# Optimization experiments

Measured on AMD Instinct MI355X. Metric: run time of the kernel, lower is better.

Reference implementation:

```python
import jax, jax.numpy as jnp
import numpy as np

T, B, C = 1024, 16, 1024
H, K, PAD = 16, 7, 6  # num_heads, kernel_size, padding_l (causal)
R = C // H


def setup_inputs() -> dict:
    key = jax.random.key(0)
    kx, kw = jax.random.split(key)
    x = jax.random.normal(kx, (T, B, C), dtype=jnp.float32)
    # xavier_uniform for weight_linear.weight of shape (H*K, C)
    bound = float(np.sqrt(6.0 / (C + H * K)))
    W = jax.random.uniform(kw, (H * K, C), dtype=jnp.float32, minval=-bound, maxval=bound)
    return {"x": x, "W": W}


def reference(x, W):
    Tn, Bn, Cn = x.shape
    # dynamic per-position conv weights: (T, B, H, K)
    w = jnp.einsum('tbc,oc->tbo', x, W).reshape(Tn, Bn, H, K)

    # band structure: row t attends absolute positions t + k - PAD, k in [0, K)
    pos = jnp.arange(Tn)[:, None] + jnp.arange(K)[None, :] - PAD     # (T, K)
    valid = (pos >= 0) & (pos < Tn)                                   # (T, K)
    logits = jnp.where(valid[:, None, None, :], w, -jnp.inf)
    wsm = jax.nn.softmax(logits, axis=-1)                             # (T, B, H, K), zeros off-band

    # windowed weighted sum (the bmm against the band matrix, done directly)
    pc = jnp.clip(pos, 0, Tn - 1)                                     # (T, K)
    xh = x.reshape(Tn, Bn, H, R)
    xg = xh[pc]                                                       # (T, K, B, H, R)
    out = jnp.einsum('tbhk,tkbhr->tbhr', wsm, xg).reshape(Tn, Bn, Cn)

    # dense (B*H, T, T) softmaxed band matrix, as returned by the torch module
    w_bht = wsm.transpose(1, 2, 0, 3).reshape(Bn * H, Tn, K)
    dense = jnp.zeros((Bn * H, Tn, Tn), wsm.dtype)
    dense = dense.at[:, jnp.arange(Tn)[:, None], pc].add(jnp.where(valid, w_bht, 0.0))
    return out, dense
```

## Files before the change

kernel.cpp:

```cpp
#include <hip/hip_runtime.h>
#include <math.h>

#define TT 1024
#define BB 16
#define CC 1024
#define HH 16
#define KK 7
#define PADL 6
#define HK 112
#define LSTRIDE 116

typedef short bf16x8 __attribute__((ext_vector_type(8)));
typedef float f32x4 __attribute__((ext_vector_type(4)));

__device__ __forceinline__ short f2bf(float f) {
    union { float f; unsigned u; } v; v.f = f;
    unsigned r = v.u + 0x7fff + ((v.u >> 16) & 1);
    return (short)(r >> 16);
}

__global__ __launch_bounds__(256) void k0_cvtW(const float* __restrict__ W,
                                               short* __restrict__ Wb) {
    const int i = (blockIdx.x * 256 + threadIdx.x) * 8;
    const float4 a0 = *(const float4*)(W + i);
    const float4 a1 = *(const float4*)(W + i + 4);
    bf16x8 v;
    v[0] = f2bf(a0.x); v[1] = f2bf(a0.y); v[2] = f2bf(a0.z); v[3] = f2bf(a0.w);
    v[4] = f2bf(a1.x); v[5] = f2bf(a1.y); v[6] = f2bf(a1.z); v[7] = f2bf(a1.w);
    *(bf16x8*)(Wb + i) = v;
}

__global__ __launch_bounds__(256) void k1_mfma(const float* __restrict__ x,
                                               const short* __restrict__ Wb,
                                               float* __restrict__ wsm) {
    __shared__ __align__(16) float Llog[4][16 * LSTRIDE];
    __shared__ __align__(16) float Lout[4][16 * HK];

    const int tid = threadIdx.x;
    const int w = tid >> 6;
    const int lane = tid & 63;
    const int quad = lane >> 4;
    const int lr = lane & 15;
    const int strip = blockIdx.x * 4 + w;
    const int r0 = strip * 16;

    bf16x8 ap, bp;
#pragma unroll
    for (int e = 0; e < 8; ++e) {
        const int k = quad * 8 + e;
        ap[e] = (k == lr) ? (short)0x3F80 : (short)0;
        bp[e] = f2bf((float)k);
    }
    f32x4 pz = (f32x4){0.f, 0.f, 0.f, 0.f};
    pz = __builtin_amdgcn_mfma_f32_16x16x32_bf16(ap, bp, pz, 0, 0, 0);
    const bool claim = (pz[0] == (float)(quad * 4)) &&
                       (pz[1] == (float)(quad * 4 + 1));

    const float* __restrict__ xa = x + (size_t)(r0 + lr) * CC + quad * 8;
    const short* __restrict__ wb = Wb + (size_t)lr * CC + quad * 8;

    f32x4 acc[7];
#pragma unroll
    for (int j = 0; j < 7; ++j) acc[j] = (f32x4){0.f, 0.f, 0.f, 0.f};

#pragma unroll 4
    for (int k0 = 0; k0 < CC; k0 += 32) {
        const float4 a0 = *(const float4*)(xa + k0);
        const float4 a1 = *(const float4*)(xa + k0 + 4);
        bf16x8 af;
        af[0] = f2bf(a0.x); af[1] = f2bf(a0.y); af[2] = f2bf(a0.z); af[3] = f2bf(a0.w);
        af[4] = f2bf(a1.x); af[5] = f2bf(a1.y); af[6] = f2bf(a1.z); af[7] = f2bf(a1.w);
#pragma unroll
        for (int j = 0; j < 7; ++j) {
            const bf16x8 bfrag = *(const bf16x8*)(wb + (size_t)(j * 16) * CC + k0);
            acc[j] = __builtin_amdgcn_mfma_f32_16x16x32_bf16(af, bfrag, acc[j], 0, 0, 0);
        }
    }

#pragma unroll
    for (int j = 0; j < 7; ++j)
#pragma unroll
        for (int r = 0; r < 4; ++r) {
            const int rowi = claim ? (quad * 4 + r) : lr;
            const int coli = claim ? lr : (quad * 4 + r);
            Llog[w][rowi * LSTRIDE + j * 16 + coli] = acc[j][r];
        }
    __syncthreads();

    const int kmin = (strip >= PADL) ? 0 : (PADL - strip);
#pragma unroll
    for (int p = 0; p < 4; ++p) {
        const int idx = p * 64 + lane;
        const int m = idx >> 4;
        const int h = idx & 15;
        const float* lp = &Llog[w][m * LSTRIDE + h * KK];
        float a[KK];
#pragma unroll
        for (int k = 0; k < KK; ++k) a[k] = lp[k];

        float mx = -INFINITY;
#pragma unroll
        for (int k = 0; k < KK; ++k)
            if (k >= kmin) mx = fmaxf(mx, a[k]);
        float e[KK], s = 0.f;
#pragma unroll
        for (int k = 0; k < KK; ++k) {
            if (k >= kmin) { e[k] = expf(a[k] - mx); s += e[k]; }
            else           { e[k] = 0.f; }
        }
        const float inv = 1.f / s;
        float* op = &Lout[w][m * HK + h * KK];
#pragma unroll
        for (int k = 0; k < KK; ++k) op[k] = e[k] * inv;
    }
    __syncthreads();

    float* __restrict__ dst = wsm + (size_t)r0 * HK;
    const float* __restrict__ src = &Lout[w][0];
#pragma unroll
    for (int i = 0; i < 7; ++i) {
        const int o = i * 256 + lane * 4;
        *(float4*)(dst + o) = *(const float4*)(src + o);
    }
}

__global__ __launch_bounds__(256) void k23_fused(const float* __restrict__ x,
                                                 const float* __restrict__ wsm,
                                                 float* __restrict__ dense,
                                                 float* __restrict__ out) {
    const int tid = threadIdx.x;
    const int base = blockIdx.x * 10;

    for (int it = 0; it < 10; ++it) {
        const int blk = base + it;

        if ((blk % 5) == 0) {
            const int r0 = (blk / 5) << 2;
            const int t = r0 >> 4;
            const int c = tid << 2;
            const int h = c >> 6;
            const int kmin = (t >= PADL) ? 0 : (PADL - t);

#pragma unroll
            for (int i = 0; i < 4; ++i) {
                const int row = r0 + i;
                const float* __restrict__ wp =
                    wsm + ((size_t)row * HH + h) * KK;
                float w[KK];
#pragma unroll
                for (int k = 0; k < KK; ++k) w[k] = wp[k];

                f32x4 acc = (f32x4){0.f, 0.f, 0.f, 0.f};
                for (int k = kmin; k < KK; ++k) {
                    const f32x4 xv = *(const f32x4*)(
                        x + ((size_t)row + (size_t)(k - PADL) * BB) * CC + c);
                    acc[0] += w[k] * xv[0];
                    acc[1] += w[k] * xv[1];
                    acc[2] += w[k] * xv[2];
                    acc[3] += w[k] * xv[3];
                }
                __builtin_nontemporal_store(acc,
                    (f32x4*)(out + (size_t)row * CC + c));
            }
        } else {
            const int blk2 = blk - (blk / 5) - 1;
            const int bh = blk2 >> 6;
            const int tc = blk2 & 63;
            const int b = bh >> 4;
            const int h = bh & 15;
            const int t0 = tc * 16;

            const int col = tid << 2;
            float* __restrict__ drow =
                dense + ((size_t)bh * TT + t0) * TT + col;

#pragma unroll
            for (int i = 0; i < 16; ++i) {
                const int t = t0 + i;
                const int lo = t - PADL;
                f32x4 v = (f32x4){0.f, 0.f, 0.f, 0.f};
                if (col + 3 >= lo && col <= t) {
                    const float* __restrict__ wp =
                        wsm + (((size_t)t * BB + b) * HH + h) * KK;
#pragma unroll
                    for (int j = 0; j < 4; ++j) {
                        const int cc = col + j;
                        if (cc >= lo && cc <= t && cc >= 0)
                            v[j] = wp[cc - lo];
                    }
                }
                __builtin_nontemporal_store(v, (f32x4*)drow);
                drow += TT;
            }
        }
    }
}

extern "C" void kernel_launch(void* const* d_in, const int* in_sizes, int n_in,
                              void* d_out, int out_size, void* d_ws, size_t ws_size,
                              hipStream_t stream) {
    const float* x = (const float*)d_in[0];
    const float* W = (const float*)d_in[1];
    float* out = (float*)d_out;
    float* dense = out + (size_t)TT * BB * CC;
    float* wsm = (float*)d_ws;
    short* Wb = (short*)(wsm + (size_t)TT * BB * HK);

    k0_cvtW<<<56, 256, 0, stream>>>(W, Wb);
    k1_mfma<<<256, 256, 0, stream>>>(x, Wb, wsm);
    k23_fused<<<2048, 256, 0, stream>>>(x, wsm, dense, out);
}
```

Baseline: 1.203 ms.

## Assign one (batch,head) dense slab per block and stage band weights in LDS

```diff
diff --git a/kernel.cpp b/kernel.cpp
--- a/kernel.cpp
+++ b/kernel.cpp
@@ -128,71 +128,67 @@
                                                  const float* __restrict__ wsm,
                                                  float* __restrict__ dense,
                                                  float* __restrict__ out) {
+    __shared__ float Lband[TT][8];
     const int tid = threadIdx.x;
-    const int base = blockIdx.x * 10;
-
-    for (int it = 0; it < 10; ++it) {
-        const int blk = base + it;
-
-        if ((blk % 5) == 0) {
-            const int r0 = (blk / 5) << 2;
-            const int t = r0 >> 4;
-            const int c = tid << 2;
-            const int h = c >> 6;
-            const int kmin = (t >= PADL) ? 0 : (PADL - t);
-
-#pragma unroll
-            for (int i = 0; i < 4; ++i) {
-                const int row = r0 + i;
-                const float* __restrict__ wp =
-                    wsm + ((size_t)row * HH + h) * KK;
-                float w[KK];
-#pragma unroll
-                for (int k = 0; k < KK; ++k) w[k] = wp[k];
-
-                f32x4 acc = (f32x4){0.f, 0.f, 0.f, 0.f};
-                for (int k = kmin; k < KK; ++k) {
-                    const f32x4 xv = *(const f32x4*)(
-                        x + ((size_t)row + (size_t)(k - PADL) * BB) * CC + c);
-                    acc[0] += w[k] * xv[0];
-                    acc[1] += w[k] * xv[1];
-                    acc[2] += w[k] * xv[2];
-                    acc[3] += w[k] * xv[3];
-                }
-                __builtin_nontemporal_store(acc,
-                    (f32x4*)(out + (size_t)row * CC + c));
+    const int bh = blockIdx.x;
+    const int b = bh >> 4;
+    const int h = bh & 15;
+
+#pragma unroll 2
+    for (int q = 0; q < 16; ++q) {
+        const int item = bh * 16 + q;
+        const int r0 = item << 2;
+        const int t = r0 >> 4;
+        const int c = tid << 2;
+        const int hh = c >> 6;
+        const int kmin = (t >= PADL) ? 0 : (PADL - t);
+
+#pragma unroll
+        for (int i = 0; i < 4; ++i) {
+            const int row = r0 + i;
+            const float* __restrict__ wp = wsm + ((size_t)row * HH + hh) * KK;
+            float w[KK];
+#pragma unroll
+            for (int k = 0; k < KK; ++k) w[k] = wp[k];
+
+            f32x4 acc = (f32x4){0.f, 0.f, 0.f, 0.f};
+            for (int k = kmin; k < KK; ++k) {
+                const f32x4 xv = *(const f32x4*)(
+                    x + ((size_t)row + (size_t)(k - PADL) * BB) * CC + c);
+                acc[0] += w[k] * xv[0];
+                acc[1] += w[k] * xv[1];
+                acc[2] += w[k] * xv[2];
+                acc[3] += w[k] * xv[3];
             }
-        } else {
-            const int blk2 = blk - (blk / 5) - 1;
-            const int bh = blk2 >> 6;
-            const int tc = blk2 & 63;
-            const int b = bh >> 4;
-            const int h = bh & 15;
-            const int t0 = tc * 16;
-
-            const int col = tid << 2;
-            float* __restrict__ drow =
-                dense + ((size_t)bh * TT + t0) * TT + col;
-
-#pragma unroll
-            for (int i = 0; i < 16; ++i) {
-                const int t = t0 + i;
-                const int lo = t - PADL;
-                f32x4 v = (f32x4){0.f, 0.f, 0.f, 0.f};
-                if (col + 3 >= lo && col <= t) {
-                    const float* __restrict__ wp =
-                        wsm + (((size_t)t * BB + b) * HH + h) * KK;
-#pragma unroll
-                    for (int j = 0; j < 4; ++j) {
-                        const int cc = col + j;
-                        if (cc >= lo && cc <= t && cc >= 0)
-                            v[j] = wp[cc - lo];
-                    }
-                }
-                __builtin_nontemporal_store(v, (f32x4*)drow);
-                drow += TT;
+            __builtin_nontemporal_store(acc,
+                (f32x4*)(out + (size_t)row * CC + c));
+        }
+    }
+
+    for (int idx = tid; idx < TT * KK; idx += 256) {
+        const int t = idx / KK;
+        const int j = idx - t * KK;
+        Lband[t][j] = wsm[(((size_t)t * BB + b) * HH + h) * KK + j];
+    }
+    __syncthreads();
+
+    const int col = tid << 2;
+    float* __restrict__ drow = dense + ((size_t)bh << 20) + col;
+
+#pragma unroll 4
+    for (int t = 0; t < TT; ++t) {
+        const int lo = t - PADL;
+        f32x4 v = (f32x4){0.f, 0.f, 0.f, 0.f};
+        if (col + 3 >= lo && col <= t) {
+#pragma unroll
+            for (int j = 0; j < 4; ++j) {
+                const int cc = col + j;
+                if (cc >= lo && cc <= t && cc >= 0)
+                    v[j] = Lband[t][cc - lo];
             }
         }
+        __builtin_nontemporal_store(v, (f32x4*)drow);
+        drow += TT;
     }
 }
 
@@ -208,5 +204,5 @@
 
     k0_cvtW<<<56, 256, 0, stream>>>(W, Wb);
     k1_mfma<<<256, 256, 0, stream>>>(x, Wb, wsm);
-    k23_fused<<<2048, 256, 0, stream>>>(x, wsm, dense, out);
-}
+    k23_fused<<<256, 256, 0, stream>>>(x, wsm, dense, out);
+}
```

New measurement: 1.294 ms. 1.08x slower.
